# Kernel optimization log

Measured on AMD Instinct MI355X. Metric: run time of the kernel, lower is better.

Reference implementation:

```python
import jax, jax.numpy as jnp
import numpy as np

WS = 11  # window_size
PS = 16  # patch_size

def _gauss(ws, sigma=1.5):
    x = np.arange(ws) - ws // 2
    g = np.exp(-(x.astype(np.float64) ** 2) / (2.0 * sigma ** 2))
    return (g / g.sum()).astype(np.float32)

def _window(ws, channel):
    g = _gauss(ws)
    w2 = np.outer(g, g)[None, None]  # (1,1,ws,ws)
    return jnp.asarray(np.broadcast_to(w2, (channel, 1, ws, ws)).copy())

def _conv(x, w, groups=1, pad=0):
    return jax.lax.conv_general_dilated(
        x, w, (1, 1), ((pad, pad), (pad, pad)),
        feature_group_count=groups,
        dimension_numbers=('NCHW', 'OIHW', 'NCHW'))

def expand_patches(mask, ps):
    B, C, H, W = mask.shape
    # per-patch max-pool
    small = mask.reshape(B, C, H // ps, ps, W // ps, ps).max(axis=(3, 5))
    kernel = jnp.ones((1, 1, 3, 3), jnp.float32)
    dil = (_conv(small, kernel, 1, 1) > 0).astype(jnp.float32)
    # nearest-neighbor upsample back to (H, W) == repeat by ps
    return jnp.repeat(jnp.repeat(dil, ps, axis=2), ps, axis=3)

def setup_inputs() -> dict:
    key = jax.random.key(0)
    k1, k2, k3 = jax.random.split(key, 3)
    B, C, H, W = 16, 3, 512, 512
    img1 = jax.random.uniform(k1, (B, C, H, W), jnp.float32)
    img2 = jax.random.uniform(k2, (B, C, H, W), jnp.float32)
    mask = jax.random.randint(k3, (B, 1, H, W), 0, 2).astype(jnp.int32)
    return {"img1": img1, "img2": img2, "mask": mask}

def reference(img1, img2, mask):
    C = img1.shape[1]
    window = _window(WS, C)  # (C,1,WS,WS)
    maskf = expand_patches(mask.astype(jnp.float32), PS)
    # val_range auto-detection (data-dependent, as in the torch code)
    max_val = jnp.where(jnp.max(img1) > 128, 255.0, 1.0)
    min_val = jnp.where(jnp.min(img1) < -0.5, -1.0, 0.0)
    L = max_val - min_val
    # groups=1 conv of 1-channel mask with (C,1,WS,WS) weight -> C output channels
    valid = (_conv(maskf, window, 1) == 1).astype(img1.dtype)
    mu1 = _conv(img1, window, C)
    mu2 = _conv(img2, window, C)
    mu1_sq = mu1 * mu1
    mu2_sq = mu2 * mu2
    mu1_mu2 = mu1 * mu2
    sigma1_sq = _conv(img1 * img1, window, C) - mu1_sq
    sigma2_sq = _conv(img2 * img2, window, C) - mu2_sq
    sigma12 = _conv(img1 * img2, window, C) - mu1_mu2
    C1 = (0.01 * L) ** 2
    C2 = (0.03 * L) ** 2
    v1 = 2.0 * sigma12 + C2
    v2 = sigma1_sq + sigma2_sq + C2
    ssim_map = (2.0 * mu1_mu2 + C1) * v1 / ((mu1_sq + mu2_sq + C1) * v2)
    return jnp.mean(ssim_map * valid)
```

## Files before the change

kernel.cpp:

```cpp
#include <hip/hip_runtime.h>
#include <cmath>
#include <cstdint>
#include <cstring>

#define OUTD 502
#define TSX  64
#define TSY  32
#define HT2P   20
#define NTAP 11
#define GX   8
#define GY   16
#define NPARTIAL (48 * GY * GX)

typedef float    f32x2 __attribute__((ext_vector_type(2)));
typedef float    f32x4 __attribute__((ext_vector_type(4)));
typedef _Float16 f16x4 __attribute__((ext_vector_type(4)));
typedef _Float16 f16x8 __attribute__((ext_vector_type(8)));
typedef __attribute__((address_space(3))) const _Float16 lds_cf16;

struct GW { float g[NTAP]; float cm; };

__device__ __forceinline__ f32x4 mfma_f16(f16x8 a, f16x8 b, f32x4 c) {
    return __builtin_amdgcn_mfma_f32_16x16x32_f16(a, b, c, 0, 0, 0);
}

__global__ __launch_bounds__(256) void patch_max_kernel(const int* __restrict__ mask,
                                                        int* __restrict__ smallbuf) {
    const int py = blockIdx.x;
    const int b  = blockIdx.y;
    const int tid = threadIdx.x;
    const int lane = tid & 63, wv = tid >> 6;
    const int4* m4 = (const int4*)(mask + ((size_t)b << 18) + (size_t)py * 16 * 512);
    #pragma unroll
    for (int j = 0; j < 8; ++j) {
        int px  = wv + 4 * j;
        int row = lane >> 2, q = lane & 3;
        int4 v = m4[row * 128 + px * 4 + q];
        int mx = max(max(v.x, v.y), max(v.z, v.w));
        #pragma unroll
        for (int off = 32; off >= 1; off >>= 1) mx = max(mx, __shfl_xor(mx, off));
        if (lane == 0) smallbuf[((b << 5) + py) * 32 + px] = mx;
    }
}

__global__ __launch_bounds__(256) void ssim_kernel(const float* __restrict__ img1,
                                                   const float* __restrict__ img2,
                                                   const int* __restrict__ smallbuf,
                                                   float* __restrict__ partial, GW gw) {
    __shared__ __align__(16) _Float16 sHT[4][48][HT2P];
    __shared__ _Float16 gpad[48];
    __shared__ int sdil[15];
    __shared__ float wsum[4];

    const int tid  = threadIdx.x;
    const int wv   = tid >> 6, lane = tid & 63;
    const int nidx = lane & 15, quad = lane >> 4;
    const int x0 = blockIdx.x * TSX, y0 = blockIdx.y * TSY;
    const int bc = blockIdx.z;
    const size_t base = (size_t)bc << 18;

    const int cb = 16 * wv;

    int gxc = x0 + cb + quad * 8; gxc = gxc > 504 ? 504 : gxc;
    f16x8 fa[3], fb[3];
    #pragma unroll
    for (int h = 0; h < 3; ++h) {
        int gy = y0 + 16 * h + nidx; gy = gy > 511 ? 511 : gy;
        const float* p1 = img1 + base + ((size_t)gy << 9) + gxc;
        const float* p2 = img2 + base + ((size_t)gy << 9) + gxc;
        f32x4 alo = *(const f32x4*)p1, ahi = *(const f32x4*)(p1 + 4);
        f32x4 blo = *(const f32x4*)p2, bhi = *(const f32x4*)(p2 + 4);
        f16x4 al = __builtin_convertvector(alo, f16x4);
        f16x4 ah = __builtin_convertvector(ahi, f16x4);
        f16x4 bl = __builtin_convertvector(blo, f16x4);
        f16x4 bh = __builtin_convertvector(bhi, f16x4);
        fa[h] = __builtin_shufflevector(al, ah, 0, 1, 2, 3, 4, 5, 6, 7);
        fb[h] = __builtin_shufflevector(bl, bh, 0, 1, 2, 3, 4, 5, 6, 7);
    }

    if (tid < 48) {
        int k = tid - 15;
        int kc = k < 0 ? 0 : (k > 10 ? 10 : k);
        gpad[tid] = (k == kc) ? (_Float16)gw.g[kc] : (_Float16)0.f;
    }

    if (tid >= 192 && tid < 207) {
        int t = tid - 192;
        int tr = t / 5, tc = t - tr * 5;
        int pr = 2 * (int)blockIdx.y + tr;
        int pc = (int)blockIdx.x * 4 + tc;
        int acc = 0;
        if (pr < 32 && pc < 32) {
            const int* sb = smallbuf + ((bc / 3) << 10);
            #pragma unroll
            for (int dy = -1; dy <= 1; ++dy)
                #pragma unroll
                for (int dx = -1; dx <= 1; ++dx) {
                    int ny = pr + dy, nx = pc + dx;
                    if (ny >= 0 && ny < 32 && nx >= 0 && nx < 32) acc |= sb[(ny << 5) + nx];
                }
        }
        sdil[t] = acc ? 1 : 0;
    }
    __syncthreads();

    f16x8 af;
    {
        const _Float16* gp = &gpad[quad * 8 - nidx + 15];
        #pragma unroll
        for (int j = 0; j < 8; ++j) af[j] = gp[j];
    }

    _Float16* wp = &sHT[wv][nidx][quad * 4];
    lds_cf16* rp = (lds_cf16*)&sHT[wv][8 * quad + (nidx >> 2)][4 * (nidx & 3)];

    f32x4 acca[4], accb[4];
    #pragma unroll
    for (int mm = 0; mm < 4; ++mm) {
        f16x8 f0, f1, f2;
        if (mm == 0)      { f0 = fa[0]; f1 = fa[1]; f2 = fa[2]; }
        else if (mm == 1) { f0 = fb[0]; f1 = fb[1]; f2 = fb[2]; }
        else if (mm == 2) { f0 = fa[0] * fb[0]; f1 = fa[1] * fb[1]; f2 = fa[2] * fb[2]; }
        else              { f0 = fa[0] * fa[0] + fb[0] * fb[0];
                            f1 = fa[1] * fa[1] + fb[1] * fb[1];
                            f2 = fa[2] * fa[2] + fb[2] * fb[2]; }
        f32x4 z = {0.f, 0.f, 0.f, 0.f};
        f32x4 c0 = mfma_f16(af, f0, z);
        f32x4 c1 = mfma_f16(af, f1, z);
        f32x4 c2 = mfma_f16(af, f2, z);
        *(f16x4*)(wp)       = __builtin_convertvector(c0, f16x4);
        *(f16x4*)(wp + 320) = __builtin_convertvector(c1, f16x4);
        *(f16x4*)(wp + 640) = __builtin_convertvector(c2, f16x4);
        f16x4 r0, r1, r2, r3;
        asm volatile("ds_read_b64_tr_b16 %0, %4 offset:0\n\t"
                     "ds_read_b64_tr_b16 %1, %4 offset:160\n\t"
                     "ds_read_b64_tr_b16 %2, %4 offset:640\n\t"
                     "ds_read_b64_tr_b16 %3, %4 offset:800"
                     : "=&v"(r0), "=&v"(r1), "=&v"(r2), "=&v"(r3)
                     : "v"(rp) : "memory");
        asm volatile("s_waitcnt lgkmcnt(0)" ::: "memory");
        __builtin_amdgcn_sched_barrier(0);
        f16x8 hba = __builtin_shufflevector(r0, r1, 0, 1, 2, 3, 4, 5, 6, 7);
        f16x8 hbb = __builtin_shufflevector(r2, r3, 0, 1, 2, 3, 4, 5, 6, 7);
        acca[mm] = mfma_f16(af, hba, z);
        accb[mm] = mfma_f16(af, hbb, z);
    }

    const float C1v = 1e-4f, C2v = 9e-4f;
    const float cm = gw.cm;
    float lsum = 0.f;
    {
        const int xl = cb + nidx;
        const int x = x0 + xl;
        if (x < OUTD) {
            const int lc0 = xl >> 4, lc1 = (xl + 10) >> 4;
            const int p0 = sdil[lc0]      & sdil[lc1];
            const int p1 = sdil[5 + lc0]  & sdil[5 + lc1];
            const int p2 = sdil[10 + lc0] & sdil[10 + lc1];

            #pragma unroll
            for (int r = 0; r < 4; ++r) {
                int q4r = quad * 4 + r;
                int cond = q4r < 6;
                int va = cond ? p0 : (p0 & p1);
                int yb = y0 + 16 + q4r;
                int vb = cond ? p1 : (p1 & p2);
                vb = (yb < OUTD) ? vb : 0;
                f32x2 mu1 = {acca[0][r], accb[0][r]};
                f32x2 mu2 = {acca[1][r], accb[1][r]};
                f32x2 Sab = {acca[2][r], accb[2][r]};
                f32x2 Sss = {acca[3][r], accb[3][r]};
                mu1 *= cm; mu2 *= cm; Sab *= cm; Sss *= cm;
                f32x2 mu1s = mu1 * mu1, mu2s = mu2 * mu2, mu12 = mu1 * mu2;
                f32x2 sg12 = Sab - mu12;
                f32x2 sigS = Sss - mu1s - mu2s;
                f32x2 num = (2.f * mu12 + C1v) * (2.f * sg12 + C2v);
                f32x2 den = (mu1s + mu2s + C1v) * (sigS + C2v);
                if (va) lsum += __fdividef(num[0], den[0]);
                if (vb) lsum += __fdividef(num[1], den[1]);
            }
        }
    }

    #pragma unroll
    for (int off = 32; off >= 1; off >>= 1) lsum += __shfl_xor(lsum, off);
    if ((tid & 63) == 0) wsum[tid >> 6] = lsum;
    __syncthreads();
    if (tid == 0)
        partial[((int)blockIdx.z * GY + (int)blockIdx.y) * GX + (int)blockIdx.x] =
            wsum[0] + wsum[1] + wsum[2] + wsum[3];
}

__global__ __launch_bounds__(256) void finalize_kernel(const float* __restrict__ partial,
                                                       float* __restrict__ out) {
    __shared__ double sd[256];
    double s = 0.0;
    const f32x4* p4 = (const f32x4*)partial;
    for (int i = threadIdx.x; i < NPARTIAL / 4; i += 256) {
        f32x4 vv = p4[i];
        s += (double)vv.x + (double)vv.y + (double)vv.z + (double)vv.w;
    }
    sd[threadIdx.x] = s;
    __syncthreads();
    for (int st = 128; st >= 1; st >>= 1) {
        if (threadIdx.x < st) sd[threadIdx.x] += sd[threadIdx.x + st];
        __syncthreads();
    }
    if (threadIdx.x == 0) out[0] = (float)(sd[0] / 12096192.0);
}

static inline float fp16_rtne(double x) {
    float f = (float)x;
    uint32_t u; memcpy(&u, &f, 4);
    u = (u + 0xFFFu + ((u >> 13) & 1u)) & ~0x1FFFu;
    memcpy(&f, &u, 4);
    return f;
}

extern "C" void kernel_launch(void* const* d_in, const int* in_sizes, int n_in,
                              void* d_out, int out_size, void* d_ws, size_t ws_size,
                              hipStream_t stream) {
    const float* img1 = (const float*)d_in[0];
    const float* img2 = (const float*)d_in[1];
    const int*   mask = (const int*)d_in[2];
    float* out = (float*)d_out;

    char* ws = (char*)d_ws;
    float* partial  = (float*)ws;
    int*   smallbuf = (int*)(ws + NPARTIAL * 4);

    GW gw;
    double gd[NTAP], gsum = 0.0;
    for (int i = 0; i < NTAP; ++i) {
        double x = (double)(i - 5);
        gd[i] = exp(-(x * x) / 4.5);
        gsum += gd[i];
    }
    double wsumr = 0.0;
    for (int i = 0; i < NTAP; ++i) {
        gw.g[i] = fp16_rtne(gd[i] / gsum);
        wsumr += (double)gw.g[i];
    }
    gw.cm = (float)(1.0 / (wsumr * wsumr));

    patch_max_kernel<<<dim3(32, 16), 256, 0, stream>>>(mask, smallbuf);
    ssim_kernel<<<dim3(GX, GY, 48), 256, 0, stream>>>(img1, img2, smallbuf, partial, gw);
    finalize_kernel<<<1, 256, 0, stream>>>(partial, out);
}
```

Before: 166.3 us.

## Fuse mask patch-max and final reduction into single SSIM kernel

Removes the separate patch-max and finalize kernels. Each SSIM block now reads its 7x5 neighborhood of mask patches directly and does the max and dilation in shared memory. The last block to finish, detected with an atomic counter, performs the final double-precision reduction. This saves two kernel launches and their serialization gaps. In exchange, mask reads are redundant across blocks (each mask patch is reread by many blocks and by all 3 channels), and a memset plus an atomic counter are added.

```diff
diff --git a/kernel.cpp b/kernel.cpp
--- a/kernel.cpp
+++ b/kernel.cpp
@@ -11,6 +11,7 @@
 #define GX   8
 #define GY   16
 #define NPARTIAL (48 * GY * GX)
+#define TOTBLK NPARTIAL
 
 typedef float    f32x2 __attribute__((ext_vector_type(2)));
 typedef float    f32x4 __attribute__((ext_vector_type(4)));
@@ -24,33 +25,19 @@
     return __builtin_amdgcn_mfma_f32_16x16x32_f16(a, b, c, 0, 0, 0);
 }
 
-__global__ __launch_bounds__(256) void patch_max_kernel(const int* __restrict__ mask,
-                                                        int* __restrict__ smallbuf) {
-    const int py = blockIdx.x;
-    const int b  = blockIdx.y;
-    const int tid = threadIdx.x;
-    const int lane = tid & 63, wv = tid >> 6;
-    const int4* m4 = (const int4*)(mask + ((size_t)b << 18) + (size_t)py * 16 * 512);
-    #pragma unroll
-    for (int j = 0; j < 8; ++j) {
-        int px  = wv + 4 * j;
-        int row = lane >> 2, q = lane & 3;
-        int4 v = m4[row * 128 + px * 4 + q];
-        int mx = max(max(v.x, v.y), max(v.z, v.w));
-        #pragma unroll
-        for (int off = 32; off >= 1; off >>= 1) mx = max(mx, __shfl_xor(mx, off));
-        if (lane == 0) smallbuf[((b << 5) + py) * 32 + px] = mx;
-    }
-}
-
-__global__ __launch_bounds__(256) void ssim_kernel(const float* __restrict__ img1,
-                                                   const float* __restrict__ img2,
-                                                   const int* __restrict__ smallbuf,
-                                                   float* __restrict__ partial, GW gw) {
+__global__ __launch_bounds__(256) void ssim_fused(const float* __restrict__ img1,
+                                                  const float* __restrict__ img2,
+                                                  const int* __restrict__ mask,
+                                                  float* __restrict__ partial,
+                                                  unsigned int* __restrict__ counter,
+                                                  float* __restrict__ out, GW gw) {
     __shared__ __align__(16) _Float16 sHT[4][48][HT2P];
     __shared__ _Float16 gpad[48];
+    __shared__ int pm[35];
     __shared__ int sdil[15];
     __shared__ float wsum[4];
+    __shared__ int lastflag;
+    __shared__ double sd[256];
 
     const int tid  = threadIdx.x;
     const int wv   = tid >> 6, lane = tid & 63;
@@ -78,29 +65,43 @@
         fb[h] = __builtin_shufflevector(bl, bh, 0, 1, 2, 3, 4, 5, 6, 7);
     }
 
-    if (tid < 48) {
-        int k = tid - 15;
+    if (tid < 35) pm[tid] = 0;
+    else if (tid >= 64 && tid < 112) {
+        int t = tid - 64;
+        int k = t - 15;
         int kc = k < 0 ? 0 : (k > 10 ? 10 : k);
-        gpad[tid] = (k == kc) ? (_Float16)gw.g[kc] : (_Float16)0.f;
-    }
-
-    if (tid >= 192 && tid < 207) {
-        int t = tid - 192;
-        int tr = t / 5, tc = t - tr * 5;
-        int pr = 2 * (int)blockIdx.y + tr;
-        int pc = (int)blockIdx.x * 4 + tc;
+        gpad[t] = (k == kc) ? (_Float16)gw.g[kc] : (_Float16)0.f;
+    } else if (tid == 192) lastflag = 0;
+    __syncthreads();
+
+    {
+        const int* mbase = mask + ((size_t)(bc / 3) << 18);
+        #pragma unroll
+        for (int T = tid; T < 560; T += 256) {
+            int p = T >> 4, i = T & 15;
+            int pr = 2 * (int)blockIdx.y - 1 + p / 7;
+            int pc = 4 * (int)blockIdx.x - 1 + p % 7;
+            if (pr >= 0 && pr < 32 && pc >= 0 && pc < 32) {
+                const int4* r4 = (const int4*)(mbase + (((pr << 4) + i) << 9) + (pc << 4));
+                int4 v0 = r4[0], v1 = r4[1], v2 = r4[2], v3 = r4[3];
+                int m = max(max(max(v0.x, v0.y), max(v0.z, v0.w)),
+                            max(max(v1.x, v1.y), max(v1.z, v1.w)));
+                m = max(m, max(max(max(v2.x, v2.y), max(v2.z, v2.w)),
+                               max(max(v3.x, v3.y), max(v3.z, v3.w))));
+                if (m) atomicMax(&pm[p], 1);
+            }
+        }
+    }
+    __syncthreads();
+
+    if (tid < 15) {
+        int tr = tid / 5, tc = tid - tr * 5;
         int acc = 0;
-        if (pr < 32 && pc < 32) {
-            const int* sb = smallbuf + ((bc / 3) << 10);
+        #pragma unroll
+        for (int dy = 0; dy < 3; ++dy)
             #pragma unroll
-            for (int dy = -1; dy <= 1; ++dy)
-                #pragma unroll
-                for (int dx = -1; dx <= 1; ++dx) {
-                    int ny = pr + dy, nx = pc + dx;
-                    if (ny >= 0 && ny < 32 && nx >= 0 && nx < 32) acc |= sb[(ny << 5) + nx];
-                }
-        }
-        sdil[t] = acc ? 1 : 0;
+            for (int dx = 0; dx < 3; ++dx) acc |= pm[(tr + dy) * 7 + tc + dx];
+        sdil[tid] = acc ? 1 : 0;
     }
     __syncthreads();
 
@@ -186,27 +187,31 @@
     for (int off = 32; off >= 1; off >>= 1) lsum += __shfl_xor(lsum, off);
     if ((tid & 63) == 0) wsum[tid >> 6] = lsum;
     __syncthreads();
-    if (tid == 0)
+    if (tid == 0) {
         partial[((int)blockIdx.z * GY + (int)blockIdx.y) * GX + (int)blockIdx.x] =
             wsum[0] + wsum[1] + wsum[2] + wsum[3];
-}
-
-__global__ __launch_bounds__(256) void finalize_kernel(const float* __restrict__ partial,
-                                                       float* __restrict__ out) {
-    __shared__ double sd[256];
-    double s = 0.0;
-    const f32x4* p4 = (const f32x4*)partial;
-    for (int i = threadIdx.x; i < NPARTIAL / 4; i += 256) {
-        f32x4 vv = p4[i];
-        s += (double)vv.x + (double)vv.y + (double)vv.z + (double)vv.w;
-    }
-    sd[threadIdx.x] = s;
-    __syncthreads();
-    for (int st = 128; st >= 1; st >>= 1) {
-        if (threadIdx.x < st) sd[threadIdx.x] += sd[threadIdx.x + st];
+        __threadfence();
+        unsigned int old = atomicAdd(counter, 1u);
+        if (old == TOTBLK - 1) lastflag = 1;
+    }
+    __syncthreads();
+
+    if (lastflag) {
+        __threadfence();
+        double s = 0.0;
+        const f32x4* p4 = (const f32x4*)partial;
+        for (int i = tid; i < NPARTIAL / 4; i += 256) {
+            f32x4 vv = p4[i];
+            s += (double)vv.x + (double)vv.y + (double)vv.z + (double)vv.w;
+        }
+        sd[tid] = s;
         __syncthreads();
-    }
-    if (threadIdx.x == 0) out[0] = (float)(sd[0] / 12096192.0);
+        for (int st = 128; st >= 1; st >>= 1) {
+            if (tid < st) sd[tid] += sd[tid + st];
+            __syncthreads();
+        }
+        if (tid == 0) out[0] = (float)(sd[0] / 12096192.0);
+    }
 }
 
 static inline float fp16_rtne(double x) {
@@ -226,8 +231,8 @@
     float* out = (float*)d_out;
 
     char* ws = (char*)d_ws;
-    float* partial  = (float*)ws;
-    int*   smallbuf = (int*)(ws + NPARTIAL * 4);
+    float* partial = (float*)ws;
+    unsigned int* counter = (unsigned int*)(ws + NPARTIAL * 4);
 
     GW gw;
     double gd[NTAP], gsum = 0.0;
@@ -243,7 +248,7 @@
     }
     gw.cm = (float)(1.0 / (wsumr * wsumr));
 
-    patch_max_kernel<<<dim3(32, 16), 256, 0, stream>>>(mask, smallbuf);
-    ssim_kernel<<<dim3(GX, GY, 48), 256, 0, stream>>>(img1, img2, smallbuf, partial, gw);
-    finalize_kernel<<<1, 256, 0, stream>>>(partial, out);
-}
+    hipMemsetAsync(counter, 0, sizeof(unsigned int), stream);
+    ssim_fused<<<dim3(GX, GY, 48), 256, 0, stream>>>(img1, img2, mask,
+                                                     partial, counter, out, gw);
+}
```

New measurement: 408.7 us. 146% more time.

## Halve SSIM tile height to one 16-row output block per CTA

Applied to the files above, without the earlier changes.

Shrinks the per-block output tile from 32 to 16 rows, doubling the grid in Y, so each CTA loads 32 input rows instead of 48 and performs one vertical MFMA pass per statistic instead of two. LDS use and register pressure fall, which could raise occupancy and parallelism. The cost is more vertical halo re-reading (32 input rows per 16 output rows instead of 48 per 32), more blocks and partial sums, and a rewritten validity-mask indexing.

```diff
diff --git a/kernel.cpp b/kernel.cpp
--- a/kernel.cpp
+++ b/kernel.cpp
@@ -5,14 +5,13 @@
 
 #define OUTD 502
 #define TSX  64
-#define TSY  32
+#define TSY  16
 #define HT2P   20
 #define NTAP 11
 #define GX   8
-#define GY   16
+#define GY   32
 #define NPARTIAL (48 * GY * GX)
 
-typedef float    f32x2 __attribute__((ext_vector_type(2)));
 typedef float    f32x4 __attribute__((ext_vector_type(4)));
 typedef _Float16 f16x4 __attribute__((ext_vector_type(4)));
 typedef _Float16 f16x8 __attribute__((ext_vector_type(8)));
@@ -47,9 +46,9 @@
                                                    const float* __restrict__ img2,
                                                    const int* __restrict__ smallbuf,
                                                    float* __restrict__ partial, GW gw) {
-    __shared__ __align__(16) _Float16 sHT[4][48][HT2P];
+    __shared__ __align__(16) _Float16 sHT[4][32][HT2P];
     __shared__ _Float16 gpad[48];
-    __shared__ int sdil[15];
+    __shared__ int sdil[10];
     __shared__ float wsum[4];
 
     const int tid  = threadIdx.x;
@@ -62,9 +61,9 @@
     const int cb = 16 * wv;
 
     int gxc = x0 + cb + quad * 8; gxc = gxc > 504 ? 504 : gxc;
-    f16x8 fa[3], fb[3];
-    #pragma unroll
-    for (int h = 0; h < 3; ++h) {
+    f16x8 fa[2], fb[2];
+    #pragma unroll
+    for (int h = 0; h < 2; ++h) {
         int gy = y0 + 16 * h + nidx; gy = gy > 511 ? 511 : gy;
         const float* p1 = img1 + base + ((size_t)gy << 9) + gxc;
         const float* p2 = img2 + base + ((size_t)gy << 9) + gxc;
@@ -84,11 +83,10 @@
         gpad[tid] = (k == kc) ? (_Float16)gw.g[kc] : (_Float16)0.f;
     }
 
-    if (tid >= 192 && tid < 207) {
+    if (tid >= 192 && tid < 202) {
         int t = tid - 192;
-        int tr = t / 5, tc = t - tr * 5;
-        int pr = 2 * (int)blockIdx.y + tr;
-        int pc = (int)blockIdx.x * 4 + tc;
+        int pr = (int)blockIdx.y + (t >= 5 ? 1 : 0);
+        int pc = (int)blockIdx.x * 4 + (t >= 5 ? t - 5 : t);
         int acc = 0;
         if (pr < 32 && pc < 32) {
             const int* sb = smallbuf + ((bc / 3) << 10);
@@ -114,36 +112,29 @@
     _Float16* wp = &sHT[wv][nidx][quad * 4];
     lds_cf16* rp = (lds_cf16*)&sHT[wv][8 * quad + (nidx >> 2)][4 * (nidx & 3)];
 
-    f32x4 acca[4], accb[4];
+    f32x4 acc[4];
     #pragma unroll
     for (int mm = 0; mm < 4; ++mm) {
-        f16x8 f0, f1, f2;
-        if (mm == 0)      { f0 = fa[0]; f1 = fa[1]; f2 = fa[2]; }
-        else if (mm == 1) { f0 = fb[0]; f1 = fb[1]; f2 = fb[2]; }
-        else if (mm == 2) { f0 = fa[0] * fb[0]; f1 = fa[1] * fb[1]; f2 = fa[2] * fb[2]; }
+        f16x8 f0, f1;
+        if (mm == 0)      { f0 = fa[0]; f1 = fa[1]; }
+        else if (mm == 1) { f0 = fb[0]; f1 = fb[1]; }
+        else if (mm == 2) { f0 = fa[0] * fb[0]; f1 = fa[1] * fb[1]; }
         else              { f0 = fa[0] * fa[0] + fb[0] * fb[0];
-                            f1 = fa[1] * fa[1] + fb[1] * fb[1];
-                            f2 = fa[2] * fa[2] + fb[2] * fb[2]; }
+                            f1 = fa[1] * fa[1] + fb[1] * fb[1]; }
         f32x4 z = {0.f, 0.f, 0.f, 0.f};
         f32x4 c0 = mfma_f16(af, f0, z);
         f32x4 c1 = mfma_f16(af, f1, z);
-        f32x4 c2 = mfma_f16(af, f2, z);
         *(f16x4*)(wp)       = __builtin_convertvector(c0, f16x4);
         *(f16x4*)(wp + 320) = __builtin_convertvector(c1, f16x4);
-        *(f16x4*)(wp + 640) = __builtin_convertvector(c2, f16x4);
-        f16x4 r0, r1, r2, r3;
-        asm volatile("ds_read_b64_tr_b16 %0, %4 offset:0\n\t"
-                     "ds_read_b64_tr_b16 %1, %4 offset:160\n\t"
-                     "ds_read_b64_tr_b16 %2, %4 offset:640\n\t"
-                     "ds_read_b64_tr_b16 %3, %4 offset:800"
-                     : "=&v"(r0), "=&v"(r1), "=&v"(r2), "=&v"(r3)
+        f16x4 r0, r1;
+        asm volatile("ds_read_b64_tr_b16 %0, %2 offset:0\n\t"
+                     "ds_read_b64_tr_b16 %1, %2 offset:160"
+                     : "=&v"(r0), "=&v"(r1)
                      : "v"(rp) : "memory");
         asm volatile("s_waitcnt lgkmcnt(0)" ::: "memory");
         __builtin_amdgcn_sched_barrier(0);
-        f16x8 hba = __builtin_shufflevector(r0, r1, 0, 1, 2, 3, 4, 5, 6, 7);
-        f16x8 hbb = __builtin_shufflevector(r2, r3, 0, 1, 2, 3, 4, 5, 6, 7);
-        acca[mm] = mfma_f16(af, hba, z);
-        accb[mm] = mfma_f16(af, hbb, z);
+        f16x8 hb = __builtin_shufflevector(r0, r1, 0, 1, 2, 3, 4, 5, 6, 7);
+        acc[mm] = mfma_f16(af, hb, z);
     }
 
     const float C1v = 1e-4f, C2v = 9e-4f;
@@ -154,30 +145,23 @@
         const int x = x0 + xl;
         if (x < OUTD) {
             const int lc0 = xl >> 4, lc1 = (xl + 10) >> 4;
-            const int p0 = sdil[lc0]      & sdil[lc1];
-            const int p1 = sdil[5 + lc0]  & sdil[5 + lc1];
-            const int p2 = sdil[10 + lc0] & sdil[10 + lc1];
-
+            const int vm0 = sdil[lc0] & sdil[lc1];
+            const int vm1 = vm0 & sdil[5 + lc0] & sdil[5 + lc1];
             #pragma unroll
             for (int r = 0; r < 4; ++r) {
                 int q4r = quad * 4 + r;
-                int cond = q4r < 6;
-                int va = cond ? p0 : (p0 & p1);
-                int yb = y0 + 16 + q4r;
-                int vb = cond ? p1 : (p1 & p2);
-                vb = (yb < OUTD) ? vb : 0;
-                f32x2 mu1 = {acca[0][r], accb[0][r]};
-                f32x2 mu2 = {acca[1][r], accb[1][r]};
-                f32x2 Sab = {acca[2][r], accb[2][r]};
-                f32x2 Sss = {acca[3][r], accb[3][r]};
-                mu1 *= cm; mu2 *= cm; Sab *= cm; Sss *= cm;
-                f32x2 mu1s = mu1 * mu1, mu2s = mu2 * mu2, mu12 = mu1 * mu2;
-                f32x2 sg12 = Sab - mu12;
-                f32x2 sigS = Sss - mu1s - mu2s;
-                f32x2 num = (2.f * mu12 + C1v) * (2.f * sg12 + C2v);
-                f32x2 den = (mu1s + mu2s + C1v) * (sigS + C2v);
-                if (va) lsum += __fdividef(num[0], den[0]);
-                if (vb) lsum += __fdividef(num[1], den[1]);
+                int y = y0 + q4r;
+                if (y < OUTD) {
+                    int validm = (q4r >= 6) ? vm1 : vm0;
+                    float mu1 = acc[0][r] * cm, mu2 = acc[1][r] * cm;
+                    float Sab = acc[2][r] * cm, Sss = acc[3][r] * cm;
+                    float mu1s = mu1 * mu1, mu2s = mu2 * mu2, mu12 = mu1 * mu2;
+                    float sg12 = Sab - mu12;
+                    float sigS = Sss - mu1s - mu2s;
+                    float num = (2.f * mu12 + C1v) * (2.f * sg12 + C2v);
+                    float den = (mu1s + mu2s + C1v) * (sigS + C2v);
+                    if (validm) lsum += __fdividef(num, den);
+                }
             }
         }
     }
```

Result: slower. 183.1 us (+10.1%).
